# Performance work log

Measured on AMD Instinct MI355X. Metric: run time of the kernel, lower is better.

The kernel has to match this reference:

```python
import jax, jax.numpy as jnp
import numpy as np

N, E, D_IN, D_OUT = 100000, 1600000, 64, 64


def setup_inputs() -> dict:
    key = jax.random.key(0)
    k0, k1, k2, k3 = jax.random.split(key, 4)
    x = jax.random.normal(k0, (N, D_IN), dtype=jnp.float32)
    edge_index = jax.random.randint(k1, (2, E), 0, N)  # [2, E] (src, dst)
    W = jax.random.normal(k2, (D_IN, D_OUT), dtype=jnp.float32) / np.sqrt(D_IN).astype(np.float32)
    b = jnp.zeros((D_OUT,), dtype=jnp.float32)
    causal_attention = jax.random.normal(k3, (D_OUT, D_OUT), dtype=jnp.float32)
    return {"x": x, "edge_index": edge_index, "W": W, "b": b,
            "causal_attention": causal_attention, "L": 1}


def gcn_conv(x, edge_index, W, b):
    # PyG GCNConv: x' = D^{-1/2} (A + I) D^{-1/2} (x W) + b
    n = x.shape[0]
    xw = x @ W  # [N, D_OUT]
    loops = jnp.arange(n)
    src = jnp.concatenate([edge_index[0], loops])  # [E+N]
    dst = jnp.concatenate([edge_index[1], loops])
    deg = jax.ops.segment_sum(jnp.ones_like(src, dtype=xw.dtype), dst, num_segments=n)
    dinv = jnp.where(deg > 0, jax.lax.rsqrt(deg), 0.0)
    norm = dinv[src] * dinv[dst]  # [E+N]
    agg = jax.ops.segment_sum(norm[:, None] * xw[src], dst, num_segments=n)  # [N, D_OUT]
    return agg + b


def reference(x, edge_index, W, b, causal_attention, L):
    x_conv = gcn_conv(x, edge_index, W, b)
    causal_weights = jax.nn.softmax(causal_attention, axis=1)  # row softmax
    return x_conv @ causal_weights  # [N, D_OUT]
```

## Files before the change

### kernel.cpp

```cpp
#include <hip/hip_runtime.h>
#include <hip/hip_bf16.h>


#define D 64
#define BSHIFT 6
#define BNODES 64
#define ARENA_CAP 1728
#define BIN_TILE 8192

__device__ __forceinline__ unsigned short f2bf(float f) {
    union { float f; unsigned int u; } c;
    c.f = f;
    unsigned int u = c.u;
    u += 0x7fffu + ((u >> 16) & 1u);
    return (unsigned short)(u >> 16);
}
__device__ __forceinline__ float bflo(unsigned int u) {
    union { unsigned int u; float f; } c;
    c.u = u << 16;
    return c.f;
}
__device__ __forceinline__ float bfhi(unsigned int u) {
    union { unsigned int u; float f; } c;
    c.u = u & 0xffff0000u;
    return c.f;
}

__global__ __launch_bounds__(256) void prep_kernel(const float* __restrict__ W,
                                                   const float* __restrict__ b,
                                                   const float* __restrict__ A,
                                                   float* __restrict__ M,
                                                   float* __restrict__ bs,
                                                   int* __restrict__ cursor, int nbuck) {
    __shared__ float S[D * D];
    int t = threadIdx.x;
    int gidx = blockIdx.x * 256 + t;
    if (gidx < nbuck) cursor[gidx] = gidx * ARENA_CAP;
    int wv = t >> 6, lane = t & 63;
#pragma unroll 4
    for (int rr = 0; rr < 16; rr++) {
        int r = wv * 16 + rr;
        float a = A[r * D + lane];
        float m = a;
        for (int off = 32; off; off >>= 1) m = fmaxf(m, __shfl_xor(m, off));
        float p = __expf(a - m);
        float ssum = p;
        for (int off = 32; off; off >>= 1) ssum += __shfl_xor(ssum, off);
        S[r * D + lane] = p / ssum;
    }
    __syncthreads();
    int k = blockIdx.x * 4 + wv;
    float acc = 0.f;
    for (int d2 = 0; d2 < D; d2++) acc += W[k * D + d2] * S[d2 * D + lane];
    M[k * D + lane] = acc;
    if (blockIdx.x == 0 && t < D) {
        float a2 = 0.f;
        for (int d2 = 0; d2 < D; d2++) a2 += b[d2] * S[d2 * D + t];
        bs[t] = a2;
    }
}

__global__ __launch_bounds__(512) void bin_kernel(const int* __restrict__ src,
                                                  const int* __restrict__ dst,
                                                  int* __restrict__ cursor,
                                                  int* __restrict__ binned, int E) {
    __shared__ int h[2048];
    int t = threadIdx.x;
    for (int i = t; i < 2048; i += 512) h[i] = 0;
    __syncthreads();
    int base = blockIdx.x * BIN_TILE;
    int pv[16], bk[16], rv[16];
#pragma unroll
    for (int k = 0; k < 16; k++) {
        int e = base + k * 512 + t;
        if (e < E) {
            int s = src[e], d = dst[e];
            bk[k] = (d >> BSHIFT) & 2047;
            pv[k] = (s << BSHIFT) | (d & (BNODES - 1));
            rv[k] = atomicAdd(&h[bk[k]], 1);
        }
    }
    __syncthreads();
    for (int b2 = t; b2 < 2048; b2 += 512) {
        int c = h[b2];
        if (c) h[b2] = atomicAdd(&cursor[b2], c);
    }
    __syncthreads();
#pragma unroll
    for (int k = 0; k < 16; k++) {
        int e = base + k * 512 + t;
        if (e < E) binned[h[bk[k]] + rv[k]] = pv[k];
    }
}

__global__ __launch_bounds__(256) void sort_kernel(int* __restrict__ binned,
                                                   const int* __restrict__ cursor,
                                                   int* __restrict__ rowstart,
                                                   int* __restrict__ rowend,
                                                   float* __restrict__ dinv,
                                                   int N) {
    __shared__ int buf[ARENA_CAP];
    __shared__ int h[BNODES];
    __shared__ int cur[BNODES];
    int t = threadIdx.x;
    int b = blockIdx.x;
    int s = b * ARENA_CAP;
    int cnt = cursor[b] - s;
    if (cnt > ARENA_CAP) cnt = ARENA_CAP;
    if (t < BNODES) h[t] = 0;
    __syncthreads();
    for (int i = t; i < cnt; i += 256) {
        int p = binned[s + i];
        buf[i] = p;
        atomicAdd(&h[p & (BNODES - 1)], 1);
    }
    __syncthreads();
    if (t < BNODES) {
        int v = h[t];
        int sc = v;
#pragma unroll
        for (int off = 1; off < BNODES; off <<= 1) {
            int u = __shfl_up(sc, off);
            if (t >= off) sc += u;
        }
        cur[t] = sc - v;
        int node = (b << BSHIFT) + t;
        if (node < N) {
            rowstart[node] = s + sc - v;
            rowend[node] = s + sc;
            dinv[node] = rsqrtf((float)(v + 1));
        }
    }
    __syncthreads();
    for (int i = t; i < cnt; i += 256) {
        int p = buf[i];
        int pos = atomicAdd(&cur[p & (BNODES - 1)], 1);
        binned[s + pos] = (int)((unsigned)p >> BSHIFT);
    }
}

__device__ __forceinline__ void fma4(float4& a, float xv, const float4& m) {
    a.x += xv * m.x; a.y += xv * m.y; a.z += xv * m.z; a.w += xv * m.w;
}
__global__ __launch_bounds__(256) void zmat_kernel(const float* __restrict__ x,
                                                   const float* __restrict__ M,
                                                   const float* __restrict__ dinv,
                                                   unsigned short* __restrict__ zbf,
                                                   int N) {
    __shared__ float Ms[D * D];
    __shared__ float xs[64][D + 4];
    int t = threadIdx.x;
    int row0 = blockIdx.x << 6;
    for (int i = t; i < (D * D) / 4; i += 256)
        ((float4*)Ms)[i] = ((const float4*)M)[i];
    for (int w = t; w < 1024; w += 256) {
        int r = w >> 4, c4 = (w & 15) << 2;
        int row = row0 + r;
        float4 v = make_float4(0.f, 0.f, 0.f, 0.f);
        if (row < N) v = *(const float4*)&x[(size_t)row * D + c4];
        *(float4*)&xs[r][c4] = v;
    }
    __syncthreads();
    int cg = t & 15, rg = t >> 4;
    int r0 = rg << 2, c0 = cg << 2;
    float4 a0 = make_float4(0.f, 0.f, 0.f, 0.f);
    float4 a1 = a0, a2 = a0, a3 = a0;
#pragma unroll 4
    for (int k = 0; k < D; k += 4) {
        float4 x0 = *(const float4*)&xs[r0 + 0][k];
        float4 x1 = *(const float4*)&xs[r0 + 1][k];
        float4 x2 = *(const float4*)&xs[r0 + 2][k];
        float4 x3 = *(const float4*)&xs[r0 + 3][k];
        float4 m0 = *(const float4*)&Ms[(k + 0) * D + c0];
        float4 m1 = *(const float4*)&Ms[(k + 1) * D + c0];
        float4 m2 = *(const float4*)&Ms[(k + 2) * D + c0];
        float4 m3 = *(const float4*)&Ms[(k + 3) * D + c0];
        fma4(a0, x0.x, m0); fma4(a0, x0.y, m1); fma4(a0, x0.z, m2); fma4(a0, x0.w, m3);
        fma4(a1, x1.x, m0); fma4(a1, x1.y, m1); fma4(a1, x1.z, m2); fma4(a1, x1.w, m3);
        fma4(a2, x2.x, m0); fma4(a2, x2.y, m1); fma4(a2, x2.z, m2); fma4(a2, x2.w, m3);
        fma4(a3, x3.x, m0); fma4(a3, x3.y, m1); fma4(a3, x3.z, m2); fma4(a3, x3.w, m3);
    }
    int rowb = row0 + r0;
    if (rowb < N) {
        float4 dv4 = *(const float4*)&dinv[rowb];
        ushort4 s0, s1, s2, s3;
        s0.x = f2bf(dv4.x * a0.x); s0.y = f2bf(dv4.x * a0.y);
        s0.z = f2bf(dv4.x * a0.z); s0.w = f2bf(dv4.x * a0.w);
        s1.x = f2bf(dv4.y * a1.x); s1.y = f2bf(dv4.y * a1.y);
        s1.z = f2bf(dv4.y * a1.z); s1.w = f2bf(dv4.y * a1.w);
        s2.x = f2bf(dv4.z * a2.x); s2.y = f2bf(dv4.z * a2.y);
        s2.z = f2bf(dv4.z * a2.z); s2.w = f2bf(dv4.z * a2.w);
        s3.x = f2bf(dv4.w * a3.x); s3.y = f2bf(dv4.w * a3.y);
        s3.z = f2bf(dv4.w * a3.z); s3.w = f2bf(dv4.w * a3.w);
        *(ushort4*)&zbf[(size_t)(rowb + 0) * D + c0] = s0;
        *(ushort4*)&zbf[(size_t)(rowb + 1) * D + c0] = s1;
        *(ushort4*)&zbf[(size_t)(rowb + 2) * D + c0] = s2;
        *(ushort4*)&zbf[(size_t)(rowb + 3) * D + c0] = s3;
    }
}

__global__ __launch_bounds__(256) void gather_kernel(const unsigned short* __restrict__ zbf,
                                                     const int* __restrict__ csr,
                                                     const int* __restrict__ rowstart,
                                                     const int* __restrict__ rowend,
                                                     const float* __restrict__ dinv,
                                                     const float* __restrict__ bs,
                                                     float* __restrict__ out, int n) {
    int wid = blockIdx.x * 4 + (threadIdx.x >> 6);
    int lane = threadIdx.x & 63;
    int qg = lane >> 4;
    int c4 = lane & 15;
    int stride = gridDim.x << 2;
    float4 bb = ((const float4*)bs)[c4];

    int nodeA = wid;
    int sA = 0, eA = 0;
    if (nodeA < n) { sA = rowstart[nodeA]; eA = rowend[nodeA]; }
    int nodeB = nodeA + stride;
    int sB = 0, eB = 0;
    if (nodeB < n) { sB = rowstart[nodeB]; eB = rowend[nodeB]; }
    int sregA = 0; uint2 uzA = make_uint2(0u, 0u); float diA = 0.f;
    if (nodeA < n) {
        int c0 = min(eA - sA, 64);
        if (lane < c0) sregA = csr[sA + lane];
        uzA = *(const uint2*)&zbf[(size_t)nodeA * D + 4 * c4];
        diA = dinv[nodeA];
    }

    while (nodeA < n) {
        int sregB = 0; uint2 uzB = make_uint2(0u, 0u); float diB = 0.f;
        if (nodeB < n) {
            int c0 = min(eB - sB, 64);
            if (lane < c0) sregB = csr[sB + lane];
            uzB = *(const uint2*)&zbf[(size_t)nodeB * D + 4 * c4];
            diB = dinv[nodeB];
        }
        int nodeC = nodeB + stride;
        int sC = 0, eC = 0;
        if (nodeC < n) { sC = rowstart[nodeC]; eC = rowend[nodeC]; }

        float a0 = 0.f, a1 = 0.f, a2 = 0.f, a3 = 0.f;
        int e = sA;
        bool first = true;
        while (e < eA) {
            int cnt = min(eA - e, 64);
            int sreg = sregA;
            if (!first) sreg = (lane < cnt) ? csr[e + lane] : 0;
            first = false;
            int k = 0;
            for (; k + 15 < cnt; k += 16) {
                int p0 = __shfl(sreg, k + qg);
                int p1 = __shfl(sreg, k + 4 + qg);
                int p2 = __shfl(sreg, k + 8 + qg);
                int p3 = __shfl(sreg, k + 12 + qg);
                uint2 u0 = *(const uint2*)&zbf[(size_t)p0 * D + 4 * c4];
                uint2 u1 = *(const uint2*)&zbf[(size_t)p1 * D + 4 * c4];
                uint2 u2 = *(const uint2*)&zbf[(size_t)p2 * D + 4 * c4];
                uint2 u3 = *(const uint2*)&zbf[(size_t)p3 * D + 4 * c4];
                a0 += bflo(u0.x); a1 += bfhi(u0.x); a2 += bflo(u0.y); a3 += bfhi(u0.y);
                a0 += bflo(u1.x); a1 += bfhi(u1.x); a2 += bflo(u1.y); a3 += bfhi(u1.y);
                a0 += bflo(u2.x); a1 += bfhi(u2.x); a2 += bflo(u2.y); a3 += bfhi(u2.y);
                a0 += bflo(u3.x); a1 += bfhi(u3.x); a2 += bflo(u3.y); a3 += bfhi(u3.y);
            }
            for (; k + 7 < cnt; k += 8) {
                int p0 = __shfl(sreg, k + qg);
                int p1 = __shfl(sreg, k + 4 + qg);
                uint2 u0 = *(const uint2*)&zbf[(size_t)p0 * D + 4 * c4];
                uint2 u1 = *(const uint2*)&zbf[(size_t)p1 * D + 4 * c4];
                a0 += bflo(u0.x); a1 += bfhi(u0.x); a2 += bflo(u0.y); a3 += bfhi(u0.y);
                a0 += bflo(u1.x); a1 += bfhi(u1.x); a2 += bflo(u1.y); a3 += bfhi(u1.y);
            }
            for (; k + 3 < cnt; k += 4) {
                int p0 = __shfl(sreg, k + qg);
                uint2 u0 = *(const uint2*)&zbf[(size_t)p0 * D + 4 * c4];
                a0 += bflo(u0.x); a1 += bfhi(u0.x); a2 += bflo(u0.y); a3 += bfhi(u0.y);
            }
            int r = cnt - k;
            if (r) {
                int p0 = __shfl(sreg, k + (qg < r ? qg : 0));
                uint2 u0 = *(const uint2*)&zbf[(size_t)p0 * D + 4 * c4];
                if (qg < r) {
                    a0 += bflo(u0.x); a1 += bfhi(u0.x);
                    a2 += bflo(u0.y); a3 += bfhi(u0.y);
                }
            }
            e += cnt;
        }
        a0 += __shfl_xor(a0, 16); a1 += __shfl_xor(a1, 16);
        a2 += __shfl_xor(a2, 16); a3 += __shfl_xor(a3, 16);
        a0 += __shfl_xor(a0, 32); a1 += __shfl_xor(a1, 32);
        a2 += __shfl_xor(a2, 32); a3 += __shfl_xor(a3, 32);
        if (lane < 16) {
            float4 o;
            o.x = diA * (a0 + bflo(uzA.x)) + bb.x;
            o.y = diA * (a1 + bfhi(uzA.x)) + bb.y;
            o.z = diA * (a2 + bflo(uzA.y)) + bb.z;
            o.w = diA * (a3 + bfhi(uzA.y)) + bb.w;
            *(float4*)&out[(size_t)nodeA * D + 4 * c4] = o;
        }
        nodeA = nodeB; sA = sB; eA = eB; sregA = sregB; uzA = uzB; diA = diB;
        nodeB = nodeC; sB = sC; eB = eC;
    }
}

extern "C" void kernel_launch(void* const* d_in, const int* in_sizes, int n_in,
                              void* d_out, int out_size, void* d_ws, size_t ws_size,
                              hipStream_t stream) {
    const float* x = (const float*)d_in[0];
    const int* ei = (const int*)d_in[1];
    const float* W = (const float*)d_in[2];
    const float* b = (const float*)d_in[3];
    const float* A = (const float*)d_in[4];

    const int N = in_sizes[0] / D;
    const int E = in_sizes[1] / 2;
    const int* src = ei;
    const int* dst = ei + E;
    const int NBUCK = (N + BNODES - 1) >> BSHIFT;

    char* ws = (char*)d_ws;
    size_t off = 0;
    auto alloc = [&](size_t bytes) -> char* {
        char* p = ws + off;
        off = (off + bytes + 255) & ~(size_t)255;
        return p;
    };
    int* cursor = (int*)alloc((size_t)NBUCK * 4);
    float* dinv = (float*)alloc((size_t)N * 4);
    float* M = (float*)alloc((size_t)D * D * 4);
    float* bs = (float*)alloc((size_t)D * 4);
    int* binned = (int*)alloc((size_t)NBUCK * ARENA_CAP * 4);
    int* rowstart = (int*)alloc((size_t)N * 4);
    int* rowend = (int*)alloc((size_t)N * 4);
    unsigned short* zbf = (unsigned short*)alloc((size_t)N * D * 2);
    (void)ws_size;

    prep_kernel<<<16, 256, 0, stream>>>(W, b, A, M, bs, cursor, NBUCK);
    bin_kernel<<<(E + BIN_TILE - 1) / BIN_TILE, 512, 0, stream>>>(src, dst, cursor, binned, E);
    sort_kernel<<<NBUCK, 256, 0, stream>>>(binned, cursor, rowstart, rowend, dinv, N);
    zmat_kernel<<<(N + 63) >> 6, 256, 0, stream>>>(x, M, dinv, zbf, N);
    gather_kernel<<<2048, 256, 0, stream>>>(zbf, binned, rowstart, rowend, dinv, bs, (float*)d_out, N);
}
```

Before: 171.8 us.

## Fuse per-bucket sort into gather kernel using shared-memory CSR, split degree pass

Replaces the sort kernel, which wrote sorted CSR, rowstart and rowend back to global memory, with a light degree-count kernel that only computes dinv. Each gather block now re-reads its bucket, counting-sorts it in LDS and aggregates its 64 nodes directly from the shared sorted list. This drops the global write and re-read of the sorted edge list and the row pointers. In exchange the bucket is read twice, each block uses more LDS, and the cross-node prefetch pipelining and persistent grid of the old gather kernel are gone, with a fixed 16 nodes per wave.

```diff
diff --git a/kernel.cpp b/kernel.cpp
--- a/kernel.cpp
+++ b/kernel.cpp
@@ -93,49 +93,23 @@
     }
 }
 
-__global__ __launch_bounds__(256) void sort_kernel(int* __restrict__ binned,
-                                                   const int* __restrict__ cursor,
-                                                   int* __restrict__ rowstart,
-                                                   int* __restrict__ rowend,
-                                                   float* __restrict__ dinv,
-                                                   int N) {
-    __shared__ int buf[ARENA_CAP];
+__global__ __launch_bounds__(256) void dk_kernel(const int* __restrict__ binned,
+                                                 const int* __restrict__ cursor,
+                                                 float* __restrict__ dinv, int N) {
     __shared__ int h[BNODES];
-    __shared__ int cur[BNODES];
     int t = threadIdx.x;
     int b = blockIdx.x;
-    int s = b * ARENA_CAP;
-    int cnt = cursor[b] - s;
+    int base = b * ARENA_CAP;
+    int cnt = cursor[b] - base;
     if (cnt > ARENA_CAP) cnt = ARENA_CAP;
     if (t < BNODES) h[t] = 0;
     __syncthreads();
-    for (int i = t; i < cnt; i += 256) {
-        int p = binned[s + i];
-        buf[i] = p;
-        atomicAdd(&h[p & (BNODES - 1)], 1);
-    }
+    for (int i = t; i < cnt; i += 256)
+        atomicAdd(&h[binned[base + i] & (BNODES - 1)], 1);
     __syncthreads();
     if (t < BNODES) {
-        int v = h[t];
-        int sc = v;
-#pragma unroll
-        for (int off = 1; off < BNODES; off <<= 1) {
-            int u = __shfl_up(sc, off);
-            if (t >= off) sc += u;
-        }
-        cur[t] = sc - v;
         int node = (b << BSHIFT) + t;
-        if (node < N) {
-            rowstart[node] = s + sc - v;
-            rowend[node] = s + sc;
-            dinv[node] = rsqrtf((float)(v + 1));
-        }
-    }
-    __syncthreads();
-    for (int i = t; i < cnt; i += 256) {
-        int p = buf[i];
-        int pos = atomicAdd(&cur[p & (BNODES - 1)], 1);
-        binned[s + pos] = (int)((unsigned)p >> BSHIFT);
+        if (node < N) dinv[node] = rsqrtf((float)(h[t] + 1));
     }
 }
 
@@ -199,107 +173,112 @@
     }
 }
 
-__global__ __launch_bounds__(256) void gather_kernel(const unsigned short* __restrict__ zbf,
-                                                     const int* __restrict__ csr,
-                                                     const int* __restrict__ rowstart,
-                                                     const int* __restrict__ rowend,
-                                                     const float* __restrict__ dinv,
-                                                     const float* __restrict__ bs,
-                                                     float* __restrict__ out, int n) {
-    int wid = blockIdx.x * 4 + (threadIdx.x >> 6);
-    int lane = threadIdx.x & 63;
+__global__ __launch_bounds__(256) void sg_kernel(const unsigned short* __restrict__ zbf,
+                                                 const int* __restrict__ binned,
+                                                 const int* __restrict__ cursor,
+                                                 const float* __restrict__ bs,
+                                                 float* __restrict__ out, int N) {
+    __shared__ int buf[ARENA_CAP];
+    __shared__ int srt[ARENA_CAP];
+    __shared__ int h[BNODES];
+    __shared__ int cur[BNODES];
+    __shared__ int rs[BNODES];
+    __shared__ float dv[BNODES];
+    int t = threadIdx.x;
+    int b = blockIdx.x;
+    int base = b * ARENA_CAP;
+    int cnt = cursor[b] - base;
+    if (cnt > ARENA_CAP) cnt = ARENA_CAP;
+    if (t < BNODES) h[t] = 0;
+    __syncthreads();
+    for (int i = t; i < cnt; i += 256) {
+        int p = binned[base + i];
+        buf[i] = p;
+        atomicAdd(&h[p & (BNODES - 1)], 1);
+    }
+    __syncthreads();
+    if (t < BNODES) {
+        int v = h[t];
+        int sc = v;
+#pragma unroll
+        for (int off = 1; off < BNODES; off <<= 1) {
+            int u = __shfl_up(sc, off);
+            if (t >= off) sc += u;
+        }
+        rs[t] = sc - v;
+        cur[t] = sc - v;
+        dv[t] = rsqrtf((float)(v + 1));
+    }
+    __syncthreads();
+    for (int i = t; i < cnt; i += 256) {
+        int p = buf[i];
+        int pos = atomicAdd(&cur[p & (BNODES - 1)], 1);
+        srt[pos] = (int)((unsigned)p >> BSHIFT);
+    }
+    __syncthreads();
+
+    int lane = t & 63, wv = t >> 6;
     int qg = lane >> 4;
     int c4 = lane & 15;
-    int stride = gridDim.x << 2;
     float4 bb = ((const float4*)bs)[c4];
-
-    int nodeA = wid;
-    int sA = 0, eA = 0;
-    if (nodeA < n) { sA = rowstart[nodeA]; eA = rowend[nodeA]; }
-    int nodeB = nodeA + stride;
-    int sB = 0, eB = 0;
-    if (nodeB < n) { sB = rowstart[nodeB]; eB = rowend[nodeB]; }
-    int sregA = 0; uint2 uzA = make_uint2(0u, 0u); float diA = 0.f;
-    if (nodeA < n) {
-        int c0 = min(eA - sA, 64);
-        if (lane < c0) sregA = csr[sA + lane];
-        uzA = *(const uint2*)&zbf[(size_t)nodeA * D + 4 * c4];
-        diA = dinv[nodeA];
-    }
-
-    while (nodeA < n) {
-        int sregB = 0; uint2 uzB = make_uint2(0u, 0u); float diB = 0.f;
-        if (nodeB < n) {
-            int c0 = min(eB - sB, 64);
-            if (lane < c0) sregB = csr[sB + lane];
-            uzB = *(const uint2*)&zbf[(size_t)nodeB * D + 4 * c4];
-            diB = dinv[nodeB];
-        }
-        int nodeC = nodeB + stride;
-        int sC = 0, eC = 0;
-        if (nodeC < n) { sC = rowstart[nodeC]; eC = rowend[nodeC]; }
-
+#pragma unroll 1
+    for (int nl = 0; nl < 16; nl++) {
+        int ln = wv * 16 + nl;
+        int node = (b << BSHIFT) + ln;
+        int s = rs[ln];
+        int deg = h[ln];
         float a0 = 0.f, a1 = 0.f, a2 = 0.f, a3 = 0.f;
-        int e = sA;
-        bool first = true;
-        while (e < eA) {
-            int cnt = min(eA - e, 64);
-            int sreg = sregA;
-            if (!first) sreg = (lane < cnt) ? csr[e + lane] : 0;
-            first = false;
-            int k = 0;
-            for (; k + 15 < cnt; k += 16) {
-                int p0 = __shfl(sreg, k + qg);
-                int p1 = __shfl(sreg, k + 4 + qg);
-                int p2 = __shfl(sreg, k + 8 + qg);
-                int p3 = __shfl(sreg, k + 12 + qg);
-                uint2 u0 = *(const uint2*)&zbf[(size_t)p0 * D + 4 * c4];
-                uint2 u1 = *(const uint2*)&zbf[(size_t)p1 * D + 4 * c4];
-                uint2 u2 = *(const uint2*)&zbf[(size_t)p2 * D + 4 * c4];
-                uint2 u3 = *(const uint2*)&zbf[(size_t)p3 * D + 4 * c4];
-                a0 += bflo(u0.x); a1 += bfhi(u0.x); a2 += bflo(u0.y); a3 += bfhi(u0.y);
-                a0 += bflo(u1.x); a1 += bfhi(u1.x); a2 += bflo(u1.y); a3 += bfhi(u1.y);
-                a0 += bflo(u2.x); a1 += bfhi(u2.x); a2 += bflo(u2.y); a3 += bfhi(u2.y);
-                a0 += bflo(u3.x); a1 += bfhi(u3.x); a2 += bflo(u3.y); a3 += bfhi(u3.y);
+        int k = 0;
+        for (; k + 15 < deg; k += 16) {
+            int p0 = srt[s + k + qg];
+            int p1 = srt[s + k + 4 + qg];
+            int p2 = srt[s + k + 8 + qg];
+            int p3 = srt[s + k + 12 + qg];
+            uint2 u0 = *(const uint2*)&zbf[(size_t)p0 * D + 4 * c4];
+            uint2 u1 = *(const uint2*)&zbf[(size_t)p1 * D + 4 * c4];
+            uint2 u2 = *(const uint2*)&zbf[(size_t)p2 * D + 4 * c4];
+            uint2 u3 = *(const uint2*)&zbf[(size_t)p3 * D + 4 * c4];
+            a0 += bflo(u0.x); a1 += bfhi(u0.x); a2 += bflo(u0.y); a3 += bfhi(u0.y);
+            a0 += bflo(u1.x); a1 += bfhi(u1.x); a2 += bflo(u1.y); a3 += bfhi(u1.y);
+            a0 += bflo(u2.x); a1 += bfhi(u2.x); a2 += bflo(u2.y); a3 += bfhi(u2.y);
+            a0 += bflo(u3.x); a1 += bfhi(u3.x); a2 += bflo(u3.y); a3 += bfhi(u3.y);
+        }
+        for (; k + 7 < deg; k += 8) {
+            int p0 = srt[s + k + qg];
+            int p1 = srt[s + k + 4 + qg];
+            uint2 u0 = *(const uint2*)&zbf[(size_t)p0 * D + 4 * c4];
+            uint2 u1 = *(const uint2*)&zbf[(size_t)p1 * D + 4 * c4];
+            a0 += bflo(u0.x); a1 += bfhi(u0.x); a2 += bflo(u0.y); a3 += bfhi(u0.y);
+            a0 += bflo(u1.x); a1 += bfhi(u1.x); a2 += bflo(u1.y); a3 += bfhi(u1.y);
+        }
+        for (; k + 3 < deg; k += 4) {
+            int p0 = srt[s + k + qg];
+            uint2 u0 = *(const uint2*)&zbf[(size_t)p0 * D + 4 * c4];
+            a0 += bflo(u0.x); a1 += bfhi(u0.x); a2 += bflo(u0.y); a3 += bfhi(u0.y);
+        }
+        int r = deg - k;
+        if (r) {
+            int p0 = srt[s + k + (qg < r ? qg : 0)];
+            uint2 u0 = *(const uint2*)&zbf[(size_t)p0 * D + 4 * c4];
+            if (qg < r) {
+                a0 += bflo(u0.x); a1 += bfhi(u0.x);
+                a2 += bflo(u0.y); a3 += bfhi(u0.y);
             }
-            for (; k + 7 < cnt; k += 8) {
-                int p0 = __shfl(sreg, k + qg);
-                int p1 = __shfl(sreg, k + 4 + qg);
-                uint2 u0 = *(const uint2*)&zbf[(size_t)p0 * D + 4 * c4];
-                uint2 u1 = *(const uint2*)&zbf[(size_t)p1 * D + 4 * c4];
-                a0 += bflo(u0.x); a1 += bfhi(u0.x); a2 += bflo(u0.y); a3 += bfhi(u0.y);
-                a0 += bflo(u1.x); a1 += bfhi(u1.x); a2 += bflo(u1.y); a3 += bfhi(u1.y);
-            }
-            for (; k + 3 < cnt; k += 4) {
-                int p0 = __shfl(sreg, k + qg);
-                uint2 u0 = *(const uint2*)&zbf[(size_t)p0 * D + 4 * c4];
-                a0 += bflo(u0.x); a1 += bfhi(u0.x); a2 += bflo(u0.y); a3 += bfhi(u0.y);
-            }
-            int r = cnt - k;
-            if (r) {
-                int p0 = __shfl(sreg, k + (qg < r ? qg : 0));
-                uint2 u0 = *(const uint2*)&zbf[(size_t)p0 * D + 4 * c4];
-                if (qg < r) {
-                    a0 += bflo(u0.x); a1 += bfhi(u0.x);
-                    a2 += bflo(u0.y); a3 += bfhi(u0.y);
-                }
-            }
-            e += cnt;
         }
         a0 += __shfl_xor(a0, 16); a1 += __shfl_xor(a1, 16);
         a2 += __shfl_xor(a2, 16); a3 += __shfl_xor(a3, 16);
         a0 += __shfl_xor(a0, 32); a1 += __shfl_xor(a1, 32);
         a2 += __shfl_xor(a2, 32); a3 += __shfl_xor(a3, 32);
-        if (lane < 16) {
+        if (lane < 16 && node < N) {
+            uint2 uz = *(const uint2*)&zbf[(size_t)node * D + 4 * c4];
+            float di = dv[ln];
             float4 o;
-            o.x = diA * (a0 + bflo(uzA.x)) + bb.x;
-            o.y = diA * (a1 + bfhi(uzA.x)) + bb.y;
-            o.z = diA * (a2 + bflo(uzA.y)) + bb.z;
-            o.w = diA * (a3 + bfhi(uzA.y)) + bb.w;
-            *(float4*)&out[(size_t)nodeA * D + 4 * c4] = o;
-        }
-        nodeA = nodeB; sA = sB; eA = eB; sregA = sregB; uzA = uzB; diA = diB;
-        nodeB = nodeC; sB = sC; eB = eC;
+            o.x = di * (a0 + bflo(uz.x)) + bb.x;
+            o.y = di * (a1 + bfhi(uz.x)) + bb.y;
+            o.z = di * (a2 + bflo(uz.y)) + bb.z;
+            o.w = di * (a3 + bfhi(uz.y)) + bb.w;
+            *(float4*)&out[(size_t)node * D + 4 * c4] = o;
+        }
     }
 }
 
@@ -330,14 +309,12 @@
     float* M = (float*)alloc((size_t)D * D * 4);
     float* bs = (float*)alloc((size_t)D * 4);
     int* binned = (int*)alloc((size_t)NBUCK * ARENA_CAP * 4);
-    int* rowstart = (int*)alloc((size_t)N * 4);
-    int* rowend = (int*)alloc((size_t)N * 4);
     unsigned short* zbf = (unsigned short*)alloc((size_t)N * D * 2);
     (void)ws_size;
 
     prep_kernel<<<16, 256, 0, stream>>>(W, b, A, M, bs, cursor, NBUCK);
     bin_kernel<<<(E + BIN_TILE - 1) / BIN_TILE, 512, 0, stream>>>(src, dst, cursor, binned, E);
-    sort_kernel<<<NBUCK, 256, 0, stream>>>(binned, cursor, rowstart, rowend, dinv, N);
+    dk_kernel<<<NBUCK, 256, 0, stream>>>(binned, cursor, dinv, N);
     zmat_kernel<<<(N + 63) >> 6, 256, 0, stream>>>(x, M, dinv, zbf, N);
-    gather_kernel<<<2048, 256, 0, stream>>>(zbf, binned, rowstart, rowend, dinv, bs, (float*)d_out, N);
-}
+    sg_kernel<<<NBUCK, 256, 0, stream>>>(zbf, binned, cursor, bs, (float*)d_out, N);
+}
```

After: 167.9 us. 1.02x faster.
